# Kernel tuning notes

Hardware: AMD Instinct MI355X
Metric: run time of the kernel (lower is better)

The kernel has to match this reference:

```python
import jax, jax.numpy as jnp
import numpy as np

D_MODEL = 1024
H = 16
D_K = D_MODEL // H
NEG = -1e9


def setup_inputs() -> dict:
    key = jax.random.key(0)
    ks = jax.random.split(key, 8)
    B, S = 4, 2048
    q = jax.random.normal(ks[0], (B, S, D_MODEL), dtype=jnp.float32)
    k = jax.random.normal(ks[1], (B, S, D_MODEL), dtype=jnp.float32)
    v = jax.random.normal(ks[2], (B, S, D_MODEL), dtype=jnp.float32)
    mask = jax.random.randint(ks[3], (B, S), 0, 2, dtype=jnp.int32)
    scale = 1.0 / np.sqrt(D_MODEL)
    Wq = jax.random.normal(ks[4], (D_MODEL, D_MODEL), dtype=jnp.float32) * scale
    Wk = jax.random.normal(ks[5], (D_MODEL, D_MODEL), dtype=jnp.float32) * scale
    Wv = jax.random.normal(ks[6], (D_MODEL, D_MODEL), dtype=jnp.float32) * scale
    Wo = jax.random.normal(ks[7], (D_MODEL, D_MODEL), dtype=jnp.float32) * scale
    return {"q": q, "k": k, "v": v, "mask": mask,
            "Wq": Wq, "Wk": Wk, "Wv": Wv, "Wo": Wo}


def _split_heads(x):
    # [B,S,d_model] -> [B,H,S,d_k]
    B, S, _ = x.shape
    return x.reshape(B, S, H, D_K).transpose(0, 2, 1, 3)


def reference(q, k, v, mask, Wq, Wk, Wv, Wo):
    # Linear projections (torch Linear: x @ W.T, no bias)
    query = _split_heads(jnp.einsum('bsd,ed->bse', q, Wq))
    key_ = _split_heads(jnp.einsum('bsd,ed->bse', k, Wk))
    value = _split_heads(jnp.einsum('bsd,ed->bse', v, Wv))
    # scaled dot-product attention, manual path
    scores = jnp.einsum('bhqd,bhkd->bhqk', query, key_) / jnp.sqrt(
        jnp.asarray(D_K, dtype=query.dtype))
    m = (mask == 0)[:, None, None, :]  # [B,1,1,S]
    scores = jnp.where(m, jnp.asarray(NEG, dtype=scores.dtype), scores)
    attn = jax.nn.softmax(scores, axis=-1)
    mh = jnp.einsum('bhqk,bhkd->bhqd', attn, value)
    # merge heads -> [B,S,d_model]
    B = mh.shape[0]
    mh = mh.transpose(0, 2, 1, 3).reshape(B, -1, D_MODEL)
    return jnp.einsum('bsd,ed->bse', mh, Wo)
```

## Files before the change

kernel.cpp:

```cpp
#include <hip/hip_runtime.h>
#include <math.h>

typedef __attribute__((ext_vector_type(4))) float f32x4;
typedef __attribute__((ext_vector_type(8))) __bf16 bf16x8;
typedef __attribute__((ext_vector_type(2))) __bf16 bf16x2;

#ifndef __has_builtin
#define __has_builtin(x) 0
#endif

#if __has_builtin(__builtin_amdgcn_exp2f)
#define EXP2F(x) __builtin_amdgcn_exp2f(x)
#else
#define EXP2F(x) exp2f(x)
#endif

__device__ __forceinline__ ushort f2bf(float f) {
  return (ushort)((__float_as_uint(f) + 0x8000u) >> 16);
}

__device__ __forceinline__ uint pack_bf16(float a, float b) {
#if __has_builtin(__builtin_amdgcn_cvt_pk_bf16_f32)
  bf16x2 p = __builtin_amdgcn_cvt_pk_bf16_f32(a, b);
  return __builtin_bit_cast(uint, p);
#elif __has_builtin(__builtin_amdgcn_perm)
  uint au = __float_as_uint(a) + 0x8000u;
  uint bu = __float_as_uint(b) + 0x8000u;
  return __builtin_amdgcn_perm(bu, au, 0x07060302u);
#else
  return (uint)f2bf(a) | ((uint)f2bf(b) << 16);
#endif
}

__device__ __forceinline__ void async_cp16(const void* g, void* l) {
  __builtin_amdgcn_global_load_lds(
      (const __attribute__((address_space(1))) void*)g,
      (__attribute__((address_space(3))) void*)l, 16, 0, 0);
}


__global__ __launch_bounds__(256) void prep_kernel(
    const float* __restrict__ q, const float* __restrict__ k, const float* __restrict__ v,
    const float* __restrict__ Wq, const float* __restrict__ Wk, const float* __restrict__ Wv,
    const float* __restrict__ Wo, const int* __restrict__ mask,
    ushort* qb, ushort* kb, ushort* vb,
    ushort* wqb, ushort* wkb, ushort* wvb, ushort* wob,
    float* bias) {
  int b = blockIdx.x;
  int tid = threadIdx.x;
  if (b < 4096) {
    int j = b >> 10;
    const float* in = j == 0 ? Wq : (j == 1 ? Wk : (j == 2 ? Wv : Wo));
    ushort* out = j == 0 ? wqb : (j == 1 ? wkb : (j == 2 ? wvb : wob));
    int i = (b & 1023) * 256 + tid;
    float4 f = ((const float4*)in)[i];
    uint2 o;
    o.x = pack_bf16(f.x, f.y);
    o.y = pack_bf16(f.z, f.w);
    ((uint2*)out)[i] = o;
  } else if (b < 28672) {
    int bb = b - 4096;
    int j = bb >> 13;
    const float* in = j == 0 ? q : (j == 1 ? k : v);
    ushort* out = j == 0 ? qb : (j == 1 ? kb : vb);
    int i = (bb & 8191) * 256 + tid;
    float4 f = ((const float4*)in)[i];
    uint2 o;
    o.x = pack_bf16(f.x, f.y);
    o.y = pack_bf16(f.z, f.w);
    ((uint2*)out)[i] = o;
  } else {
    int i = (b - 28672) * 256 + tid;
    bias[i] = mask[i] ? 0.0f : -1e9f;
  }
}


__device__ __forceinline__ void gemm_body(const ushort* __restrict__ A,
                                          const ushort* __restrict__ W,
                                          void* __restrict__ Cout, int mode,
                                          int bm, int bn) {
  constexpr int N = 1024, K = 1024;
  constexpr int NT = K / 64;
  __shared__ ushort As[2][128 * 64];
  __shared__ ushort Bs[2][128 * 64];
  const int tid = threadIdx.x;
  const int w = tid >> 6, lane = tid & 63;
  const int g = lane >> 4, cc = lane & 15;
  const int wm = (w >> 1) * 64, wn = (w & 1) * 64;

  f32x4 acc[4][4];
#pragma unroll
  for (int i = 0; i < 4; ++i)
#pragma unroll
    for (int j = 0; j < 4; ++j) acc[i][j] = (f32x4)0.0f;

  auto stage = [&](int k0, int buf) {
#pragma unroll
    for (int j = 0; j < 4; ++j) {
      int cbase = w * 256 + j * 64;
      int cid = cbase + lane;
      int row = cid & 127, kb = cid >> 7;
      async_cp16(A + (size_t)(bm + row) * K + k0 + kb * 8, &As[buf][cbase * 8]);
      async_cp16(W + (size_t)(bn + row) * K + k0 + kb * 8, &Bs[buf][cbase * 8]);
    }
  };

  auto compute = [&](int cur) {
#pragma unroll
    for (int ks = 0; ks < 2; ++ks) {
      bf16x8 af[4], bfr[4];
#pragma unroll
      for (int mi = 0; mi < 4; ++mi)
        af[mi] = *(const bf16x8*)&As[cur][((ks * 4 + g) * 128 + wm + mi * 16 + cc) * 8];
#pragma unroll
      for (int ni = 0; ni < 4; ++ni)
        bfr[ni] = *(const bf16x8*)&Bs[cur][((ks * 4 + g) * 128 + wn + ni * 16 + cc) * 8];
      __builtin_amdgcn_s_setprio(1);
#pragma unroll
      for (int mi = 0; mi < 4; ++mi)
#pragma unroll
        for (int ni = 0; ni < 4; ++ni)
          acc[mi][ni] =
              __builtin_amdgcn_mfma_f32_16x16x32_bf16(af[mi], bfr[ni], acc[mi][ni], 0, 0, 0);
      __builtin_amdgcn_s_setprio(0);
    }
  };

  stage(0, 0);
  stage(64, 1);
  for (int it = 0; it < NT - 1; ++it) {
    const int cur = it & 1;
    asm volatile("s_waitcnt vmcnt(8)" ::: "memory");
    __builtin_amdgcn_s_barrier();
    __builtin_amdgcn_sched_barrier(0);
    compute(cur);
    __builtin_amdgcn_sched_barrier(0);
    __builtin_amdgcn_s_barrier();
    __builtin_amdgcn_sched_barrier(0);
    if (it < NT - 2) stage((it + 2) * 64, cur);
  }
  asm volatile("s_waitcnt vmcnt(0)" ::: "memory");
  __builtin_amdgcn_s_barrier();
  __builtin_amdgcn_sched_barrier(0);
  compute((NT - 1) & 1);

  const float qsc = 0.18033688011112042f;
#pragma unroll
  for (int mi = 0; mi < 4; ++mi) {
#pragma unroll
    for (int ni = 0; ni < 4; ++ni) {
#pragma unroll
      for (int r = 0; r < 4; ++r) {
        int row = bm + wm + mi * 16 + g * 4 + r;
        int col = bn + wn + ni * 16 + cc;
        float val = acc[mi][ni][r];
        if (mode == 0) {
          ((ushort*)Cout)[(size_t)row * N + col] = f2bf(val);
        } else if (mode == 1) {
          ((float*)Cout)[(size_t)row * N + col] = val;
        } else if (mode == 3) {
          ((ushort*)Cout)[(size_t)row * N + col] = f2bf(val * qsc);
        } else {
          int b = row >> 11, s = row & 2047;
          int h = col >> 6, d = col & 63;
          ((ushort*)Cout)[(size_t)((b * 16 + h) * 64 + d) * 2048 + s] = f2bf(val);
        }
      }
    }
  }
}

__device__ __forceinline__ void swz_tile(int* bm, int* bn) {
  int l = blockIdx.x + (blockIdx.y << 3);
  int t = ((l & 7) << 6) + (l >> 3);
  *bn = (t & 7) * 128;
  *bm = (t >> 3) * 128;
}

__global__ __launch_bounds__(256) void qkv_gemm_kernel(const ushort* qb, const ushort* kb,
                                                       const ushort* vb, const ushort* wq,
                                                       const ushort* wk, const ushort* wv,
                                                       ushort* Qp, ushort* Kp, ushort* Vt) {
  int z = blockIdx.z;
  const ushort* A = z == 0 ? qb : (z == 1 ? kb : vb);
  const ushort* W = z == 0 ? wq : (z == 1 ? wk : wv);
  void* C = z == 0 ? (void*)Qp : (z == 1 ? (void*)Kp : (void*)Vt);
  int bm, bn;
  swz_tile(&bm, &bn);
  gemm_body(A, W, C, z == 2 ? 2 : (z == 0 ? 3 : 0), bm, bn);
}

__global__ __launch_bounds__(256) void gemm_wo_kernel(const ushort* A, const ushort* W,
                                                      float* C) {
  int bm, bn;
  swz_tile(&bm, &bn);
  gemm_body(A, W, C, 1, bm, bn);
}

__global__ __launch_bounds__(256, 4) void attn_kernel(const ushort* __restrict__ Qp,
                                                      const ushort* __restrict__ Kp,
                                                      const ushort* __restrict__ Vt,
                                                      const float* __restrict__ bias,
                                                      ushort* __restrict__ mh) {
  constexpr int S = 2048, DM = 1024, DK = 64;
  __shared__ ushort k_lds[64 * 64];
  __shared__ ushort v_lds[64 * 64];
  __shared__ ushort pt_lds[4 * 2176];

  const int bh = blockIdx.x;
  const int qt = blockIdx.y;
  const int b = bh >> 4, h = bh & 15;
  const int tid = threadIdx.x;
  const int w = tid >> 6, lane = tid & 63;
  const int g = lane >> 4, cc = lane & 15;
  ushort* ptw = &pt_lds[w * 2176];

  const int q0 = qt * 128 + w * 32;
  bf16x8 qf[2][2];
#pragma unroll
  for (int ni = 0; ni < 2; ++ni) {
    size_t row = (size_t)(b * S + q0 + ni * 16 + cc);
#pragma unroll
    for (int ks = 0; ks < 2; ++ks)
      qf[ks][ni] = *(const bf16x8*)&Qp[row * DM + h * DK + ks * 32 + g * 8];
  }

  bf16x8 ones;
#pragma unroll
  for (int i = 0; i < 8; ++i) ones[i] = (__bf16)1.0f;

  f32x4 o_acc[4][2];
#pragma unroll
  for (int i = 0; i < 4; ++i)
#pragma unroll
    for (int j = 0; j < 2; ++j) o_acc[i][j] = (f32x4)0.0f;
  f32x4 l_acc[2] = {(f32x4)0.0f, (f32x4)0.0f};
  const float* biasb = bias + b * S;

  for (int kt = 0; kt < S / 64; ++kt) {
    if (kt) __syncthreads();
#pragma unroll
    for (int j = 0; j < 2; ++j) {
      int cb = j * 256 + w * 64;
      int cid = cb + lane;
      async_cp16(Kp + (size_t)(b * S + kt * 64 + (cid & 63)) * DM + h * DK + (cid >> 6) * 8,
                 &k_lds[cb * 8]);
      async_cp16(Vt + (size_t)(bh * DK + (cid & 63)) * S + kt * 64 + (cid >> 6) * 8,
                 &v_lds[cb * 8]);
    }
    __syncthreads();

    f32x4 sacc[4][2];
#pragma unroll
    for (int mi = 0; mi < 4; ++mi)
#pragma unroll
      for (int ni = 0; ni < 2; ++ni) sacc[mi][ni] = (f32x4)0.0f;
    __builtin_amdgcn_s_setprio(1);
#pragma unroll
    for (int ks = 0; ks < 2; ++ks)
#pragma unroll
      for (int mi = 0; mi < 4; ++mi) {
        bf16x8 kf = *(const bf16x8*)&k_lds[((ks * 4 + g) * 64 + mi * 16 + cc) * 8];
        sacc[mi][0] = __builtin_amdgcn_mfma_f32_16x16x32_bf16(kf, qf[ks][0], sacc[mi][0], 0, 0, 0);
        sacc[mi][1] = __builtin_amdgcn_mfma_f32_16x16x32_bf16(kf, qf[ks][1], sacc[mi][1], 0, 0, 0);
      }
    __builtin_amdgcn_s_setprio(0);

#pragma unroll
    for (int mi = 0; mi < 4; ++mi) {
      float4 bv = *(const float4*)&biasb[kt * 64 + mi * 16 + g * 4];
      const float* bvp = &bv.x;
#pragma unroll
      for (int ni = 0; ni < 2; ++ni) {
        float p0 = EXP2F(sacc[mi][ni][0] + bvp[0]);
        float p1 = EXP2F(sacc[mi][ni][1] + bvp[1]);
        float p2 = EXP2F(sacc[mi][ni][2] + bvp[2]);
        float p3 = EXP2F(sacc[mi][ni][3] + bvp[3]);
        uint2 pv;
        pv.x = pack_bf16(p0, p1);
        pv.y = pack_bf16(p2, p3);
        int base = ((mi * 2 + (g >> 1)) * 32 + ni * 16 + cc) * 8 + (g & 1) * 4;
        *(uint2*)&ptw[base] = pv;
      }
    }

    __builtin_amdgcn_s_setprio(1);
#pragma unroll
    for (int ks = 0; ks < 2; ++ks) {
      bf16x8 ptf[2];
#pragma unroll
      for (int ni = 0; ni < 2; ++ni)
        ptf[ni] = *(const bf16x8*)&ptw[((ks * 4 + g) * 32 + ni * 16 + cc) * 8];
      l_acc[0] = __builtin_amdgcn_mfma_f32_16x16x32_bf16(ones, ptf[0], l_acc[0], 0, 0, 0);
      l_acc[1] = __builtin_amdgcn_mfma_f32_16x16x32_bf16(ones, ptf[1], l_acc[1], 0, 0, 0);
#pragma unroll
      for (int md = 0; md < 4; ++md) {
        bf16x8 vf = *(const bf16x8*)&v_lds[((ks * 4 + g) * 64 + md * 16 + cc) * 8];
        o_acc[md][0] = __builtin_amdgcn_mfma_f32_16x16x32_bf16(vf, ptf[0], o_acc[md][0], 0, 0, 0);
        o_acc[md][1] = __builtin_amdgcn_mfma_f32_16x16x32_bf16(vf, ptf[1], o_acc[md][1], 0, 0, 0);
      }
    }
    __builtin_amdgcn_s_setprio(0);
  }

  float rl[2];
#pragma unroll
  for (int ni = 0; ni < 2; ++ni) rl[ni] = 1.0f / l_acc[ni][0];

#pragma unroll
  for (int md = 0; md < 4; ++md)
#pragma unroll
    for (int ni = 0; ni < 2; ++ni) {
      int ql = ni * 16 + cc;
      int dbase = md * 16 + g * 4;
      *(uint*)&ptw[ql * 68 + dbase] =
          pack_bf16(o_acc[md][ni][0] * rl[ni], o_acc[md][ni][1] * rl[ni]);
      *(uint*)&ptw[ql * 68 + dbase + 2] =
          pack_bf16(o_acc[md][ni][2] * rl[ni], o_acc[md][ni][3] * rl[ni]);
    }
#pragma unroll
  for (int pass = 0; pass < 4; ++pass) {
    int ql = pass * 8 + (lane >> 3);
    int dc = lane & 7;
    uint4 val = *(const uint4*)&ptw[ql * 68 + dc * 8];
    *(uint4*)&mh[(size_t)(b * S + q0 + ql) * DM + h * DK + dc * 8] = val;
  }
}


extern "C" void kernel_launch(void* const* d_in, const int* in_sizes, int n_in,
                              void* d_out, int out_size, void* d_ws, size_t ws_size,
                              hipStream_t stream) {
  const float* q = (const float*)d_in[0];
  const float* k = (const float*)d_in[1];
  const float* v = (const float*)d_in[2];
  const int* mask = (const int*)d_in[3];
  const float* Wq = (const float*)d_in[4];
  const float* Wk = (const float*)d_in[5];
  const float* Wv = (const float*)d_in[6];
  const float* Wo = (const float*)d_in[7];

  const size_t MB = 1 << 20;

  char* ws = (char*)d_ws;
  ushort* Qp = (ushort*)(ws);
  ushort* Kp = (ushort*)(ws + 16 * MB);
  ushort* Vt = (ushort*)(ws + 32 * MB);
  ushort* wqb = (ushort*)(ws + 48 * MB);
  ushort* wkb = wqb + (1 << 20);
  ushort* wvb = wkb + (1 << 20);
  ushort* wob = wvb + (1 << 20);
  float* biasbuf = (float*)(ws + 56 * MB);
  ushort* vb = (ushort*)(ws + 57 * MB);
  ushort* mh = vb;
  ushort* qb = (ushort*)d_out;
  ushort* kb = qb + (size_t)8 * 1024 * 1024;

  dim3 blk(256);

  prep_kernel<<<dim3(28704), blk, 0, stream>>>(q, k, v, Wq, Wk, Wv, Wo, mask,
                                               qb, kb, vb, wqb, wkb, wvb, wob, biasbuf);
  qkv_gemm_kernel<<<dim3(8, 64, 3), blk, 0, stream>>>(qb, kb, vb, wqb, wkb, wvb, Qp, Kp, Vt);
  attn_kernel<<<dim3(64, 16), blk, 0, stream>>>(Qp, Kp, Vt, biasbuf, mh);
  gemm_wo_kernel<<<dim3(8, 64), blk, 0, stream>>>(mh, wob, (float*)d_out);
}
```

Before: 407.9 us.

## Double-buffer K/V tiles in attention and stage bf16 mask bias in LDS

The attention kernel now double-buffers the K and V tiles in LDS and prefetches tile kt+2 while computing tile kt. Explicit vmcnt waits and barriers replace the per-tile load-then-sync pattern, with the aim of hiding global-to-LDS latency. The mask bias is stored as bf16 (0 or about -1e9) and loaded once per block into LDS, replacing per-tile float global reads. Occupancy hint drops from 4 to 3 blocks because of the extra LDS, which could reduce latency hiding across waves.

```diff
diff --git a/kernel.cpp b/kernel.cpp
--- a/kernel.cpp
+++ b/kernel.cpp
@@ -45,7 +45,7 @@
     const float* __restrict__ Wo, const int* __restrict__ mask,
     ushort* qb, ushort* kb, ushort* vb,
     ushort* wqb, ushort* wkb, ushort* wvb, ushort* wob,
-    float* bias) {
+    ushort* biasbf) {
   int b = blockIdx.x;
   int tid = threadIdx.x;
   if (b < 4096) {
@@ -71,7 +71,7 @@
     ((uint2*)out)[i] = o;
   } else {
     int i = (b - 28672) * 256 + tid;
-    bias[i] = mask[i] ? 0.0f : -1e9f;
+    biasbf[i] = mask[i] ? (ushort)0 : (ushort)0xCE6E;
   }
 }
 
@@ -198,15 +198,17 @@
   gemm_body(A, W, C, 1, bm, bn);
 }
 
-__global__ __launch_bounds__(256, 4) void attn_kernel(const ushort* __restrict__ Qp,
+__global__ __launch_bounds__(256, 3) void attn_kernel(const ushort* __restrict__ Qp,
                                                       const ushort* __restrict__ Kp,
                                                       const ushort* __restrict__ Vt,
-                                                      const float* __restrict__ bias,
+                                                      const ushort* __restrict__ biasbf,
                                                       ushort* __restrict__ mh) {
   constexpr int S = 2048, DM = 1024, DK = 64;
-  __shared__ ushort k_lds[64 * 64];
-  __shared__ ushort v_lds[64 * 64];
+  constexpr int NKT = S / 64;
+  __shared__ ushort k_lds[2][64 * 64];
+  __shared__ ushort v_lds[2][64 * 64];
   __shared__ ushort pt_lds[4 * 2176];
+  __shared__ ushort bias_lds[2048];
 
   const int bh = blockIdx.x;
   const int qt = blockIdx.y;
@@ -226,6 +228,12 @@
       qf[ks][ni] = *(const bf16x8*)&Qp[row * DM + h * DK + ks * 32 + g * 8];
   }
 
+  {
+    uint4 bvv = *(const uint4*)&biasbf[(size_t)b * S + tid * 8];
+    *(uint4*)&bias_lds[tid * 8] = bvv;
+  }
+  asm volatile("s_waitcnt lgkmcnt(0)" ::: "memory");
+
   bf16x8 ones;
 #pragma unroll
   for (int i = 0; i < 8; ++i) ones[i] = (__bf16)1.0f;
@@ -236,20 +244,30 @@
 #pragma unroll
     for (int j = 0; j < 2; ++j) o_acc[i][j] = (f32x4)0.0f;
   f32x4 l_acc[2] = {(f32x4)0.0f, (f32x4)0.0f};
-  const float* biasb = bias + b * S;
-
-  for (int kt = 0; kt < S / 64; ++kt) {
-    if (kt) __syncthreads();
+
+  auto stage = [&](int kt, int buf) {
 #pragma unroll
     for (int j = 0; j < 2; ++j) {
       int cb = j * 256 + w * 64;
       int cid = cb + lane;
       async_cp16(Kp + (size_t)(b * S + kt * 64 + (cid & 63)) * DM + h * DK + (cid >> 6) * 8,
-                 &k_lds[cb * 8]);
+                 &k_lds[buf][cb * 8]);
       async_cp16(Vt + (size_t)(bh * DK + (cid & 63)) * S + kt * 64 + (cid >> 6) * 8,
-                 &v_lds[cb * 8]);
-    }
-    __syncthreads();
+                 &v_lds[buf][cb * 8]);
+    }
+  };
+
+  stage(0, 0);
+  stage(1, 1);
+  for (int kt = 0; kt < NKT; ++kt) {
+    const int cur = kt & 1;
+    if (kt < NKT - 1) {
+      asm volatile("s_waitcnt vmcnt(4)" ::: "memory");
+    } else {
+      asm volatile("s_waitcnt vmcnt(0)" ::: "memory");
+    }
+    __builtin_amdgcn_s_barrier();
+    __builtin_amdgcn_sched_barrier(0);
 
     f32x4 sacc[4][2];
 #pragma unroll
@@ -261,7 +279,7 @@
     for (int ks = 0; ks < 2; ++ks)
 #pragma unroll
       for (int mi = 0; mi < 4; ++mi) {
-        bf16x8 kf = *(const bf16x8*)&k_lds[((ks * 4 + g) * 64 + mi * 16 + cc) * 8];
+        bf16x8 kf = *(const bf16x8*)&k_lds[cur][((ks * 4 + g) * 64 + mi * 16 + cc) * 8];
         sacc[mi][0] = __builtin_amdgcn_mfma_f32_16x16x32_bf16(kf, qf[ks][0], sacc[mi][0], 0, 0, 0);
         sacc[mi][1] = __builtin_amdgcn_mfma_f32_16x16x32_bf16(kf, qf[ks][1], sacc[mi][1], 0, 0, 0);
       }
@@ -269,8 +287,12 @@
 
 #pragma unroll
     for (int mi = 0; mi < 4; ++mi) {
-      float4 bv = *(const float4*)&biasb[kt * 64 + mi * 16 + g * 4];
-      const float* bvp = &bv.x;
+      ushort4 bw = *(const ushort4*)&bias_lds[kt * 64 + mi * 16 + g * 4];
+      float bvp[4];
+      bvp[0] = __uint_as_float((uint)bw.x << 16);
+      bvp[1] = __uint_as_float((uint)bw.y << 16);
+      bvp[2] = __uint_as_float((uint)bw.z << 16);
+      bvp[3] = __uint_as_float((uint)bw.w << 16);
 #pragma unroll
       for (int ni = 0; ni < 2; ++ni) {
         float p0 = EXP2F(sacc[mi][ni][0] + bvp[0]);
@@ -296,12 +318,19 @@
       l_acc[1] = __builtin_amdgcn_mfma_f32_16x16x32_bf16(ones, ptf[1], l_acc[1], 0, 0, 0);
 #pragma unroll
       for (int md = 0; md < 4; ++md) {
-        bf16x8 vf = *(const bf16x8*)&v_lds[((ks * 4 + g) * 64 + md * 16 + cc) * 8];
+        bf16x8 vf = *(const bf16x8*)&v_lds[cur][((ks * 4 + g) * 64 + md * 16 + cc) * 8];
         o_acc[md][0] = __builtin_amdgcn_mfma_f32_16x16x32_bf16(vf, ptf[0], o_acc[md][0], 0, 0, 0);
         o_acc[md][1] = __builtin_amdgcn_mfma_f32_16x16x32_bf16(vf, ptf[1], o_acc[md][1], 0, 0, 0);
       }
     }
     __builtin_amdgcn_s_setprio(0);
+
+    if (kt < NKT - 1) {
+      __builtin_amdgcn_sched_barrier(0);
+      __builtin_amdgcn_s_barrier();
+      __builtin_amdgcn_sched_barrier(0);
+      if (kt < NKT - 2) stage(kt + 2, cur);
+    }
   }
 
   float rl[2];
@@ -351,17 +380,16 @@
   ushort* wkb = wqb + (1 << 20);
   ushort* wvb = wkb + (1 << 20);
   ushort* wob = wvb + (1 << 20);
-  float* biasbuf = (float*)(ws + 56 * MB);
+  ushort* biasbf = (ushort*)(ws + 56 * MB);
   ushort* vb = (ushort*)(ws + 57 * MB);
   ushort* mh = vb;
   ushort* qb = (ushort*)d_out;
   ushort* kb = qb + (size_t)8 * 1024 * 1024;
 
-  dim3 blk(256);
-
-  prep_kernel<<<dim3(28704), blk, 0, stream>>>(q, k, v, Wq, Wk, Wv, Wo, mask,
-                                               qb, kb, vb, wqb, wkb, wvb, wob, biasbuf);
-  qkv_gemm_kernel<<<dim3(8, 64, 3), blk, 0, stream>>>(qb, kb, vb, wqb, wkb, wvb, Qp, Kp, Vt);
-  attn_kernel<<<dim3(64, 16), blk, 0, stream>>>(Qp, Kp, Vt, biasbuf, mh);
-  gemm_wo_kernel<<<dim3(8, 64), blk, 0, stream>>>(mh, wob, (float*)d_out);
-}
+  prep_kernel<<<dim3(28704), dim3(256), 0, stream>>>(q, k, v, Wq, Wk, Wv, Wo, mask,
+                                                     qb, kb, vb, wqb, wkb, wvb, wob, biasbf);
+  qkv_gemm_kernel<<<dim3(8, 64, 3), dim3(256), 0, stream>>>(qb, kb, vb, wqb, wkb, wvb,
+                                                            Qp, Kp, Vt);
+  attn_kernel<<<dim3(64, 16), dim3(256), 0, stream>>>(Qp, Kp, Vt, biasbf, mh);
+  gemm_wo_kernel<<<dim3(8, 64), dim3(256), 0, stream>>>(mh, wob, (float*)d_out);
+}
```

Measured after the change: 419.7 us. 1.03x slower.
